# Performance work log

Measured on AMD Instinct MI355X. Metric: run time of the kernel, lower is better.

Reference implementation:

```python
import jax, jax.numpy as jnp
import numpy as np
import math

D_IN = 1024
D_OUT = 1024
NUM_HEADS = 16
D_HEAD = D_IN // NUM_HEADS


def setup_inputs() -> dict:
    key = jax.random.key(0)
    k1, k2, k3 = jax.random.split(key, 3)
    x = jax.random.normal(k1, (4, 2048, D_IN), dtype=jnp.float32)
    W_qkv = jax.random.normal(k2, (D_IN, 3 * D_OUT), dtype=jnp.float32) * (1.0 / math.sqrt(D_IN))
    b_qkv = jax.random.normal(k3, (3 * D_OUT,), dtype=jnp.float32) * 0.01
    return {"x": x, "W_qkv": W_qkv, "b_qkv": b_qkv}


def reference(x, W_qkv, b_qkv):
    B, S, _ = x.shape
    H, Dh = NUM_HEADS, D_HEAD
    # QKV projection: [B, S, 3*d_out]
    qkv = jnp.einsum('bsd,de->bse', x, W_qkv) + b_qkv
    # reshape per original: (B, S, H, 3*Dh) -> (B, H, S, 3*Dh)
    qkv = qkv.reshape(B, S, H, 3 * Dh).transpose(0, 2, 1, 3)
    q, k, v = jnp.split(qkv, 3, axis=-1)  # each [B, H, S, Dh]
    scale = 1.0 / math.sqrt(Dh)
    scores = jnp.einsum('bhqd,bhkd->bhqk', q, k) * scale
    attn = jax.nn.softmax(scores, axis=-1)
    ctx = jnp.einsum('bhqk,bhkd->bhqd', attn, v)  # [B, H, S, Dh]
    # (B, H, S, Dh) -> (B, S, H*Dh)
    return ctx.transpose(0, 2, 1, 3).reshape(B, S, D_OUT)
```

## Files before the change

kernel.cpp:

```cpp
#include <hip/hip_runtime.h>
#include <stdint.h>
#include <math.h>

#define D_IN   1024
#define NQKV   3072
#define NHEADS 16
#define DH     64
#define BATCH  4
#define SEQ    2048
#define MTOT   (BATCH*SEQ)

typedef __bf16    bf16x8 __attribute__((ext_vector_type(8)));
typedef _Float16  f16x8  __attribute__((ext_vector_type(8)));
typedef float     f32x4  __attribute__((ext_vector_type(4)));
typedef float     f32x16 __attribute__((ext_vector_type(16)));

typedef __attribute__((address_space(3))) unsigned short       lds_us;
typedef __attribute__((address_space(1))) const unsigned short glb_us;

__device__ __forceinline__ unsigned short f2bf(float f) {
    union { float f; uint32_t u; } c; c.f = f;
    uint32_t u = c.u;
    uint32_t r = u + 0x7fffu + ((u >> 16) & 1u);
    return (unsigned short)(r >> 16);
}
__device__ __forceinline__ uint32_t pkh(float a, float b) {
    auto h = __builtin_amdgcn_cvt_pkrtz(a, b);
    uint32_t u;
    __builtin_memcpy(&u, &h, 4);
    return u;
}

__global__ void k_convert_x(const float* __restrict__ x, unsigned short* __restrict__ xb) {
    int i = blockIdx.x * 256 + threadIdx.x;
    float4 v = ((const float4*)x)[i];
    ushort4 o;
    o.x = f2bf(v.x); o.y = f2bf(v.y); o.z = f2bf(v.z); o.w = f2bf(v.w);
    ((ushort4*)xb)[i] = o;
}

__global__ void k_convert_wt(const float* __restrict__ W, unsigned short* __restrict__ Wt) {
    __shared__ float tile[32][33];
    int tx = threadIdx.x, ty = threadIdx.y;
    int n0 = blockIdx.x * 32, k0 = blockIdx.y * 32;
    #pragma unroll
    for (int i = 0; i < 4; ++i) {
        int k = k0 + ty + i*8;
        tile[ty + i*8][tx] = W[(size_t)k * NQKV + n0 + tx];
    }
    __syncthreads();
    #pragma unroll
    for (int i = 0; i < 4; ++i) {
        int n = n0 + ty + i*8;
        Wt[(size_t)n * D_IN + k0 + tx] = f2bf(tile[tx][ty + i*8]);
    }
}

__global__ __launch_bounds__(256) void k_gemm_qkv(
    const unsigned short* __restrict__ A,
    const unsigned short* __restrict__ Bt,
    const float* __restrict__ bias,
    unsigned short* __restrict__ Qb,
    unsigned short* __restrict__ Kf,
    unsigned short* __restrict__ Vf)
{
    __shared__ __align__(16) unsigned short As[128*32];
    __shared__ __align__(16) unsigned short Bs[128*32];
    const int t = threadIdx.x;
    const int wave = t >> 6, lane = t & 63, quad = lane >> 4, l15 = lane & 15;
    const int wm = wave >> 1, wn = wave & 1;
    const int m0 = blockIdx.y * 128, n0 = blockIdx.x * 128;
    const int crow = lane >> 2;
    const int ccol = (lane & 3) << 3;

    f32x4 acc[4][4] = {};
    lds_us* As3 = (lds_us*)As;
    lds_us* Bs3 = (lds_us*)Bs;

    for (int k0 = 0; k0 < D_IN; k0 += 32) {
        #pragma unroll
        for (int j = 0; j < 2; ++j) {
            int chunk = wave*2 + j;
            const unsigned short* ga = A  + (size_t)(m0 + chunk*16 + crow)*D_IN + k0 + ccol;
            const unsigned short* gb = Bt + (size_t)(n0 + chunk*16 + crow)*D_IN + k0 + ccol;
            __builtin_amdgcn_global_load_lds((glb_us*)ga, As3 + chunk*512, 16, 0, 0);
            __builtin_amdgcn_global_load_lds((glb_us*)gb, Bs3 + chunk*512, 16, 0, 0);
        }
        __syncthreads();
        bf16x8 a[4], b[4];
        #pragma unroll
        for (int tm = 0; tm < 4; ++tm)
            a[tm] = *(const bf16x8*)(&As[(wm*64 + tm*16 + l15)*32 + quad*8]);
        #pragma unroll
        for (int tn = 0; tn < 4; ++tn)
            b[tn] = *(const bf16x8*)(&Bs[(wn*64 + tn*16 + l15)*32 + quad*8]);
        #pragma unroll
        for (int tm = 0; tm < 4; ++tm)
            #pragma unroll
            for (int tn = 0; tn < 4; ++tn)
                acc[tm][tn] = __builtin_amdgcn_mfma_f32_16x16x32_bf16(a[tm], b[tn], acc[tm][tn], 0, 0, 0);
        __syncthreads();
    }
    const float qs = 0.125f * 1.44269504089f;
    #pragma unroll
    for (int tn = 0; tn < 4; ++tn) {
        const int col0 = n0 + wn*64 + tn*16;
        const int h   = col0 / 192;
        const int r0  = col0 - h*192;
        const float bv = bias[col0 + l15];
        if (r0 < 64) {
            const int dk = r0 + l15;
            #pragma unroll
            for (int tm = 0; tm < 4; ++tm)
                #pragma unroll
                for (int r = 0; r < 4; ++r) {
                    int row = m0 + wm*64 + tm*16 + quad*4 + r;
                    Qb[(size_t)row*1024 + h*64 + dk] = f2bf((acc[tm][tn][r] + bv) * qs);
                }
        } else if (r0 < 128) {
            const int dk = r0 - 64 + l15;
            const int st = dk >> 4, hi2 = (dk >> 3) & 1, j = dk & 7;
            #pragma unroll
            for (int tm = 0; tm < 4; ++tm)
                #pragma unroll
                for (int r = 0; r < 4; ++r) {
                    int row = m0 + wm*64 + tm*16 + quad*4 + r;
                    int bh = ((row >> 11) << 4) + h;
                    int chunk = (row >> 5) & 63, l31r = row & 31;
                    Kf[((size_t)(bh*64 + chunk)*4 + st)*512 + (hi2*32 + l31r)*8 + j] =
                        f2bf(acc[tm][tn][r] + bv);
                }
        } else {
            const int d = r0 - 128 + l15;
            const int dt = d >> 5, l31d = d & 31;
            #pragma unroll
            for (int tm = 0; tm < 4; ++tm)
                #pragma unroll
                for (int r = 0; r < 4; ++r) {
                    int row = m0 + wm*64 + tm*16 + quad*4 + r;
                    int bh = ((row >> 11) << 4) + h;
                    int chunk = (row >> 5) & 63;
                    int kc = row & 31, kh = kc >> 4, rem = kc & 15;
                    int hi2 = (rem >> 2) & 1;
                    int j = (rem & 3) | (((rem >> 3) & 1) << 2);
                    _Float16 hv = (_Float16)(acc[tm][tn][r] + bv);
                    Vf[(((size_t)(bh*64 + chunk)*2 + dt)*2 + kh)*512 + (hi2*32 + l31d)*8 + j] =
                        *(unsigned short*)&hv;
                }
        }
    }
}

__global__ __launch_bounds__(256) void k_attn(
    const unsigned short* __restrict__ Qb,
    const unsigned short* __restrict__ Kf,
    const unsigned short* __restrict__ Vf,
    float* __restrict__ out)
{
    const int t = threadIdx.x;
    const int wave = t >> 6, lane = t & 63;
    const int l31 = lane & 31, hi = lane >> 5;
    const int bh = blockIdx.x, b = bh >> 4, h = bh & 15;
    const int q0 = blockIdx.y * 128 + wave * 32;

    const unsigned short* qrow = Qb + (size_t)(b*SEQ + q0 + l31)*1024 + h*64;
    const unsigned short* kfb  = Kf + (size_t)bh * 64*4*512 + lane*8;
    const unsigned short* vfb  = Vf + (size_t)bh * 64*2*2*512 + lane*8;

    bf16x8 qf[4];
    #pragma unroll
    for (int st = 0; st < 4; ++st)
        qf[st] = *(const bf16x8*)(qrow + st*16 + hi*8);

    bf16x8 kf[4];
    #pragma unroll
    for (int st = 0; st < 4; ++st)
        kf[st] = *(const bf16x8*)(kfb + st*512);
    f16x8 vf[2][2];
    #pragma unroll
    for (int dt = 0; dt < 2; ++dt)
        #pragma unroll
        for (int kh = 0; kh < 2; ++kh)
            vf[dt][kh] = *(const f16x8*)(vfb + (dt*2 + kh)*512);

    f32x16 o0 = {}, o1 = {};
    float lp = 0.f;

    for (int it = 0; it < 64; ++it) {
        f32x16 s = {};
        __builtin_amdgcn_s_setprio(1);
        #pragma unroll
        for (int st = 0; st < 4; ++st)
            s = __builtin_amdgcn_mfma_f32_32x32x16_bf16(kf[st], qf[st], s, 0, 0, 0);
        __builtin_amdgcn_s_setprio(0);
        if (it < 63) {
            const unsigned short* kn = kfb + (size_t)(it+1)*4*512;
            #pragma unroll
            for (int st = 0; st < 4; ++st)
                kf[st] = *(const bf16x8*)(kn + st*512);
        }
        uint32_t w0, w1, w2, w3, w4, w5, w6, w7;
        {
            float p0, p1, p2, p3;
            p0 = exp2f(s[0]);  p1 = exp2f(s[1]);  p2 = exp2f(s[2]);  p3 = exp2f(s[3]);
            lp += (p0+p1)+(p2+p3); w0 = pkh(p0,p1); w1 = pkh(p2,p3);
            p0 = exp2f(s[4]);  p1 = exp2f(s[5]);  p2 = exp2f(s[6]);  p3 = exp2f(s[7]);
            lp += (p0+p1)+(p2+p3); w2 = pkh(p0,p1); w3 = pkh(p2,p3);
            p0 = exp2f(s[8]);  p1 = exp2f(s[9]);  p2 = exp2f(s[10]); p3 = exp2f(s[11]);
            lp += (p0+p1)+(p2+p3); w4 = pkh(p0,p1); w5 = pkh(p2,p3);
            p0 = exp2f(s[12]); p1 = exp2f(s[13]); p2 = exp2f(s[14]); p3 = exp2f(s[15]);
            lp += (p0+p1)+(p2+p3); w6 = pkh(p0,p1); w7 = pkh(p2,p3);
        }
        f16x8 pf0, pf1;
        {
            union { uint32_t u[4]; f16x8 v; } cc;
            cc.u[0] = w0; cc.u[1] = w1; cc.u[2] = w2; cc.u[3] = w3; pf0 = cc.v;
            cc.u[0] = w4; cc.u[1] = w5; cc.u[2] = w6; cc.u[3] = w7; pf1 = cc.v;
        }
        __builtin_amdgcn_s_setprio(1);
        o0 = __builtin_amdgcn_mfma_f32_32x32x16_f16(vf[0][0], pf0, o0, 0, 0, 0);
        o1 = __builtin_amdgcn_mfma_f32_32x32x16_f16(vf[1][0], pf0, o1, 0, 0, 0);
        o0 = __builtin_amdgcn_mfma_f32_32x32x16_f16(vf[0][1], pf1, o0, 0, 0, 0);
        o1 = __builtin_amdgcn_mfma_f32_32x32x16_f16(vf[1][1], pf1, o1, 0, 0, 0);
        __builtin_amdgcn_s_setprio(0);
        if (it < 63) {
            const unsigned short* vn = vfb + (size_t)(it+1)*4*512;
            #pragma unroll
            for (int dt = 0; dt < 2; ++dt)
                #pragma unroll
                for (int kh = 0; kh < 2; ++kh)
                    vf[dt][kh] = *(const f16x8*)(vn + (dt*2 + kh)*512);
        }
    }

    float lt = lp + __shfl_xor(lp, 32);
    float rl = 1.0f / lt;

    float* outb = out + (size_t)(b*SEQ + q0 + l31)*(NHEADS*DH) + h*DH + 4*hi;
    #pragma unroll
    for (int g = 0; g < 4; ++g) {
        float4 v0 = make_float4(o0[4*g]*rl, o0[4*g+1]*rl, o0[4*g+2]*rl, o0[4*g+3]*rl);
        float4 v1 = make_float4(o1[4*g]*rl, o1[4*g+1]*rl, o1[4*g+2]*rl, o1[4*g+3]*rl);
        *(float4*)(outb + 8*g)      = v0;
        *(float4*)(outb + 32 + 8*g) = v1;
    }
}

extern "C" void kernel_launch(void* const* d_in, const int* in_sizes, int n_in,
                              void* d_out, int out_size, void* d_ws, size_t ws_size,
                              hipStream_t stream) {
    const float* x    = (const float*)d_in[0];
    const float* W    = (const float*)d_in[1];
    const float* bias = (const float*)d_in[2];
    float* out = (float*)d_out;

    unsigned short* xb = (unsigned short*)d_ws;
    unsigned short* Wt = xb + (size_t)MTOT * D_IN;
    unsigned short* Qb = Wt + (size_t)NQKV * D_IN;
    unsigned short* Kf = Qb + (size_t)MTOT * D_IN;
    unsigned short* Vf = Kf + (size_t)MTOT * D_IN;

    hipLaunchKernelGGL(k_convert_x,  dim3(MTOT*D_IN/4/256), dim3(256),    0, stream, x, xb);
    hipLaunchKernelGGL(k_convert_wt, dim3(NQKV/32, D_IN/32), dim3(32, 8), 0, stream, W, Wt);
    hipLaunchKernelGGL(k_gemm_qkv,   dim3(NQKV/128, MTOT/128), dim3(256), 0, stream, xb, Wt, bias, Qb, Kf, Vf);
    hipLaunchKernelGGL(k_attn,       dim3(BATCH*NHEADS, SEQ/128), dim3(256), 0, stream, Qb, Kf, Vf, out);
}
```

Baseline: 279.5 us.

## Process two 32-row query tiles per wave to reuse K/V fragments

Each wave in the attention kernel now handles 64 query rows as two 32-row tiles that share every K and V fragment loaded from global memory. This halves K/V load traffic per query and gives the scheduler two independent MFMA/exp chains to interleave. The grid is halved to 512 blocks, and register use roughly doubles for accumulators and Q fragments, which may lower occupancy. Softmax has no max subtraction, so numerics are unchanged from before.

```diff
diff --git a/kernel.cpp b/kernel.cpp
--- a/kernel.cpp
+++ b/kernel.cpp
@@ -161,16 +161,19 @@
     const int wave = t >> 6, lane = t & 63;
     const int l31 = lane & 31, hi = lane >> 5;
     const int bh = blockIdx.x, b = bh >> 4, h = bh & 15;
-    const int q0 = blockIdx.y * 128 + wave * 32;
-
-    const unsigned short* qrow = Qb + (size_t)(b*SEQ + q0 + l31)*1024 + h*64;
+    const int q0 = blockIdx.y * 256 + wave * 64;
+
+    const unsigned short* qrowa = Qb + (size_t)(b*SEQ + q0 + l31)*1024 + h*64;
+    const unsigned short* qrowb = qrowa + (size_t)32*1024;
     const unsigned short* kfb  = Kf + (size_t)bh * 64*4*512 + lane*8;
     const unsigned short* vfb  = Vf + (size_t)bh * 64*2*2*512 + lane*8;
 
-    bf16x8 qf[4];
-    #pragma unroll
-    for (int st = 0; st < 4; ++st)
-        qf[st] = *(const bf16x8*)(qrow + st*16 + hi*8);
+    bf16x8 qfa[4], qfb4[4];
+    #pragma unroll
+    for (int st = 0; st < 4; ++st) {
+        qfa[st]  = *(const bf16x8*)(qrowa + st*16 + hi*8);
+        qfb4[st] = *(const bf16x8*)(qrowb + st*16 + hi*8);
+    }
 
     bf16x8 kf[4];
     #pragma unroll
@@ -183,15 +186,20 @@
         for (int kh = 0; kh < 2; ++kh)
             vf[dt][kh] = *(const f16x8*)(vfb + (dt*2 + kh)*512);
 
-    f32x16 o0 = {}, o1 = {};
-    float lp = 0.f;
+    f32x16 oa0 = {}, oa1 = {}, ob0 = {}, ob1 = {};
+    float lpa = 0.f, lpb = 0.f;
 
     for (int it = 0; it < 64; ++it) {
-        f32x16 s = {};
+        f32x16 sa = {}, sb = {};
         __builtin_amdgcn_s_setprio(1);
-        #pragma unroll
-        for (int st = 0; st < 4; ++st)
-            s = __builtin_amdgcn_mfma_f32_32x32x16_bf16(kf[st], qf[st], s, 0, 0, 0);
+        sa = __builtin_amdgcn_mfma_f32_32x32x16_bf16(kf[0], qfa[0],  sa, 0, 0, 0);
+        sb = __builtin_amdgcn_mfma_f32_32x32x16_bf16(kf[0], qfb4[0], sb, 0, 0, 0);
+        sa = __builtin_amdgcn_mfma_f32_32x32x16_bf16(kf[1], qfa[1],  sa, 0, 0, 0);
+        sb = __builtin_amdgcn_mfma_f32_32x32x16_bf16(kf[1], qfb4[1], sb, 0, 0, 0);
+        sa = __builtin_amdgcn_mfma_f32_32x32x16_bf16(kf[2], qfa[2],  sa, 0, 0, 0);
+        sb = __builtin_amdgcn_mfma_f32_32x32x16_bf16(kf[2], qfb4[2], sb, 0, 0, 0);
+        sa = __builtin_amdgcn_mfma_f32_32x32x16_bf16(kf[3], qfa[3],  sa, 0, 0, 0);
+        sb = __builtin_amdgcn_mfma_f32_32x32x16_bf16(kf[3], qfb4[3], sb, 0, 0, 0);
         __builtin_amdgcn_s_setprio(0);
         if (it < 63) {
             const unsigned short* kn = kfb + (size_t)(it+1)*4*512;
@@ -199,30 +207,50 @@
             for (int st = 0; st < 4; ++st)
                 kf[st] = *(const bf16x8*)(kn + st*512);
         }
-        uint32_t w0, w1, w2, w3, w4, w5, w6, w7;
         {
+            uint32_t w0, w1, w2, w3, w4, w5, w6, w7;
             float p0, p1, p2, p3;
-            p0 = exp2f(s[0]);  p1 = exp2f(s[1]);  p2 = exp2f(s[2]);  p3 = exp2f(s[3]);
-            lp += (p0+p1)+(p2+p3); w0 = pkh(p0,p1); w1 = pkh(p2,p3);
-            p0 = exp2f(s[4]);  p1 = exp2f(s[5]);  p2 = exp2f(s[6]);  p3 = exp2f(s[7]);
-            lp += (p0+p1)+(p2+p3); w2 = pkh(p0,p1); w3 = pkh(p2,p3);
-            p0 = exp2f(s[8]);  p1 = exp2f(s[9]);  p2 = exp2f(s[10]); p3 = exp2f(s[11]);
-            lp += (p0+p1)+(p2+p3); w4 = pkh(p0,p1); w5 = pkh(p2,p3);
-            p0 = exp2f(s[12]); p1 = exp2f(s[13]); p2 = exp2f(s[14]); p3 = exp2f(s[15]);
-            lp += (p0+p1)+(p2+p3); w6 = pkh(p0,p1); w7 = pkh(p2,p3);
-        }
-        f16x8 pf0, pf1;
-        {
+            p0 = exp2f(sa[0]);  p1 = exp2f(sa[1]);  p2 = exp2f(sa[2]);  p3 = exp2f(sa[3]);
+            lpa += (p0+p1)+(p2+p3); w0 = pkh(p0,p1); w1 = pkh(p2,p3);
+            p0 = exp2f(sa[4]);  p1 = exp2f(sa[5]);  p2 = exp2f(sa[6]);  p3 = exp2f(sa[7]);
+            lpa += (p0+p1)+(p2+p3); w2 = pkh(p0,p1); w3 = pkh(p2,p3);
+            p0 = exp2f(sa[8]);  p1 = exp2f(sa[9]);  p2 = exp2f(sa[10]); p3 = exp2f(sa[11]);
+            lpa += (p0+p1)+(p2+p3); w4 = pkh(p0,p1); w5 = pkh(p2,p3);
+            p0 = exp2f(sa[12]); p1 = exp2f(sa[13]); p2 = exp2f(sa[14]); p3 = exp2f(sa[15]);
+            lpa += (p0+p1)+(p2+p3); w6 = pkh(p0,p1); w7 = pkh(p2,p3);
+            f16x8 pf0, pf1;
             union { uint32_t u[4]; f16x8 v; } cc;
             cc.u[0] = w0; cc.u[1] = w1; cc.u[2] = w2; cc.u[3] = w3; pf0 = cc.v;
             cc.u[0] = w4; cc.u[1] = w5; cc.u[2] = w6; cc.u[3] = w7; pf1 = cc.v;
-        }
-        __builtin_amdgcn_s_setprio(1);
-        o0 = __builtin_amdgcn_mfma_f32_32x32x16_f16(vf[0][0], pf0, o0, 0, 0, 0);
-        o1 = __builtin_amdgcn_mfma_f32_32x32x16_f16(vf[1][0], pf0, o1, 0, 0, 0);
-        o0 = __builtin_amdgcn_mfma_f32_32x32x16_f16(vf[0][1], pf1, o0, 0, 0, 0);
-        o1 = __builtin_amdgcn_mfma_f32_32x32x16_f16(vf[1][1], pf1, o1, 0, 0, 0);
-        __builtin_amdgcn_s_setprio(0);
+            __builtin_amdgcn_s_setprio(1);
+            oa0 = __builtin_amdgcn_mfma_f32_32x32x16_f16(vf[0][0], pf0, oa0, 0, 0, 0);
+            oa1 = __builtin_amdgcn_mfma_f32_32x32x16_f16(vf[1][0], pf0, oa1, 0, 0, 0);
+            oa0 = __builtin_amdgcn_mfma_f32_32x32x16_f16(vf[0][1], pf1, oa0, 0, 0, 0);
+            oa1 = __builtin_amdgcn_mfma_f32_32x32x16_f16(vf[1][1], pf1, oa1, 0, 0, 0);
+            __builtin_amdgcn_s_setprio(0);
+        }
+        {
+            uint32_t w0, w1, w2, w3, w4, w5, w6, w7;
+            float p0, p1, p2, p3;
+            p0 = exp2f(sb[0]);  p1 = exp2f(sb[1]);  p2 = exp2f(sb[2]);  p3 = exp2f(sb[3]);
+            lpb += (p0+p1)+(p2+p3); w0 = pkh(p0,p1); w1 = pkh(p2,p3);
+            p0 = exp2f(sb[4]);  p1 = exp2f(sb[5]);  p2 = exp2f(sb[6]);  p3 = exp2f(sb[7]);
+            lpb += (p0+p1)+(p2+p3); w2 = pkh(p0,p1); w3 = pkh(p2,p3);
+            p0 = exp2f(sb[8]);  p1 = exp2f(sb[9]);  p2 = exp2f(sb[10]); p3 = exp2f(sb[11]);
+            lpb += (p0+p1)+(p2+p3); w4 = pkh(p0,p1); w5 = pkh(p2,p3);
+            p0 = exp2f(sb[12]); p1 = exp2f(sb[13]); p2 = exp2f(sb[14]); p3 = exp2f(sb[15]);
+            lpb += (p0+p1)+(p2+p3); w6 = pkh(p0,p1); w7 = pkh(p2,p3);
+            f16x8 pf0, pf1;
+            union { uint32_t u[4]; f16x8 v; } cc;
+            cc.u[0] = w0; cc.u[1] = w1; cc.u[2] = w2; cc.u[3] = w3; pf0 = cc.v;
+            cc.u[0] = w4; cc.u[1] = w5; cc.u[2] = w6; cc.u[3] = w7; pf1 = cc.v;
+            __builtin_amdgcn_s_setprio(1);
+            ob0 = __builtin_amdgcn_mfma_f32_32x32x16_f16(vf[0][0], pf0, ob0, 0, 0, 0);
+            ob1 = __builtin_amdgcn_mfma_f32_32x32x16_f16(vf[1][0], pf0, ob1, 0, 0, 0);
+            ob0 = __builtin_amdgcn_mfma_f32_32x32x16_f16(vf[0][1], pf1, ob0, 0, 0, 0);
+            ob1 = __builtin_amdgcn_mfma_f32_32x32x16_f16(vf[1][1], pf1, ob1, 0, 0, 0);
+            __builtin_amdgcn_s_setprio(0);
+        }
         if (it < 63) {
             const unsigned short* vn = vfb + (size_t)(it+1)*4*512;
             #pragma unroll
@@ -233,16 +261,22 @@
         }
     }
 
-    float lt = lp + __shfl_xor(lp, 32);
-    float rl = 1.0f / lt;
-
-    float* outb = out + (size_t)(b*SEQ + q0 + l31)*(NHEADS*DH) + h*DH + 4*hi;
+    float lta = lpa + __shfl_xor(lpa, 32);
+    float ltb = lpb + __shfl_xor(lpb, 32);
+    float rla = 1.0f / lta, rlb = 1.0f / ltb;
+
+    float* outa = out + (size_t)(b*SEQ + q0 + l31)*(NHEADS*DH) + h*DH + 4*hi;
+    float* outbp = outa + (size_t)32*(NHEADS*DH);
     #pragma unroll
     for (int g = 0; g < 4; ++g) {
-        float4 v0 = make_float4(o0[4*g]*rl, o0[4*g+1]*rl, o0[4*g+2]*rl, o0[4*g+3]*rl);
-        float4 v1 = make_float4(o1[4*g]*rl, o1[4*g+1]*rl, o1[4*g+2]*rl, o1[4*g+3]*rl);
-        *(float4*)(outb + 8*g)      = v0;
-        *(float4*)(outb + 32 + 8*g) = v1;
+        float4 v0 = make_float4(oa0[4*g]*rla, oa0[4*g+1]*rla, oa0[4*g+2]*rla, oa0[4*g+3]*rla);
+        float4 v1 = make_float4(oa1[4*g]*rla, oa1[4*g+1]*rla, oa1[4*g+2]*rla, oa1[4*g+3]*rla);
+        *(float4*)(outa + 8*g)      = v0;
+        *(float4*)(outa + 32 + 8*g) = v1;
+        float4 u0 = make_float4(ob0[4*g]*rlb, ob0[4*g+1]*rlb, ob0[4*g+2]*rlb, ob0[4*g+3]*rlb);
+        float4 u1 = make_float4(ob1[4*g]*rlb, ob1[4*g+1]*rlb, ob1[4*g+2]*rlb, ob1[4*g+3]*rlb);
+        *(float4*)(outbp + 8*g)      = u0;
+        *(float4*)(outbp + 32 + 8*g) = u1;
     }
 }
 
@@ -263,5 +297,5 @@
     hipLaunchKernelGGL(k_convert_x,  dim3(MTOT*D_IN/4/256), dim3(256),    0, stream, x, xb);
     hipLaunchKernelGGL(k_convert_wt, dim3(NQKV/32, D_IN/32), dim3(32, 8), 0, stream, W, Wt);
     hipLaunchKernelGGL(k_gemm_qkv,   dim3(NQKV/128, MTOT/128), dim3(256), 0, stream, xb, Wt, bias, Qb, Kf, Vf);
-    hipLaunchKernelGGL(k_attn,       dim3(BATCH*NHEADS, SEQ/128), dim3(256), 0, stream, Qb, Kf, Vf, out);
-}
+    hipLaunchKernelGGL(k_attn,       dim3(BATCH*NHEADS, SEQ/256), dim3(256), 0, stream, Qb, Kf, Vf, out);
+}
```

Result: faster. 272.8 us (-2.4%).
